# Optimization experiments

Hardware: AMD Instinct MI355X
Metric: run time of the kernel (lower is better)

Reference implementation:

```python
import jax, jax.numpy as jnp
import numpy as np

N, E, D, K = 50000, 600000, 128, 8
EPS = 1e-09


def setup_inputs() -> dict:
    key = jax.random.key(0)
    ks = jax.random.split(key, 10)
    feature = jax.random.normal(ks[0], (N, D), dtype=jnp.float32)
    snorm_n = jax.random.uniform(ks[1], (N, 1), dtype=jnp.float32)
    src = jax.random.randint(ks[2], (E,), 0, N, dtype=jnp.int32)
    dst = jax.random.randint(ks[3], (E,), 0, N, dtype=jnp.int32)
    W_low = jax.random.normal(ks[4], (D, D), dtype=jnp.float32) / np.sqrt(D)
    W_high = jax.random.normal(ks[5], (D, D), dtype=jnp.float32) / np.sqrt(D)
    W_mid = jax.random.normal(ks[6], (D, D), dtype=jnp.float32) / np.sqrt(D)
    gamma_low = jax.random.uniform(ks[7], (K,), dtype=jnp.float32)
    gamma_high = jax.random.uniform(ks[8], (K,), dtype=jnp.float32)
    gamma_mid = jax.random.uniform(ks[9], (K,), dtype=jnp.float32)
    bias = jnp.zeros((D,), dtype=jnp.float32)
    return {"feature": feature, "snorm_n": snorm_n, "src": src, "dst": dst,
            "W_low": W_low, "W_high": W_high, "W_mid": W_mid,
            "gamma_low": gamma_low, "gamma_high": gamma_high,
            "gamma_mid": gamma_mid, "bias": bias}


def _mp(feat, src, dst, norm):
    # symmetric-normalized SpMM: h[v] = norm[v] * sum_{u->v} norm[u]*feat[u]
    msg = (feat * norm[:, None])[src]                        # [E, D] gather
    agg = jax.ops.segment_sum(msg, dst, num_segments=N)       # [N, D] scatter-add
    return agg * norm[:, None]


def reference(feature, snorm_n, src, dst, W_low, W_high, W_mid,
              gamma_low, gamma_high, gamma_mid, bias):
    deg = jax.ops.segment_sum(jnp.ones((E,), feature.dtype), dst, num_segments=N)
    norm = jnp.clip(deg, 1.0) ** -0.5                          # in-degree^-0.5
    alpha = jnp.linspace(EPS, 1.0 - EPS, K).astype(feature.dtype)
    midalpha = jnp.linspace(EPS, 1.0, K).astype(feature.dtype)

    h = _mp(feature, src, dst, norm)

    gl = jax.nn.relu(gamma_low)
    o0 = (jnp.dot(alpha, gl) * h + jnp.dot(1.0 - alpha, gl) * feature) @ W_low.T
    gh = jax.nn.relu(gamma_high)
    o1 = (jnp.dot(-alpha, gh) * h + jnp.dot(1.0 - alpha, gh) * feature) @ W_high.T
    gm = jax.nn.relu(gamma_mid)
    h1 = _mp(h, src, dst, norm)
    o2 = (jnp.sum(gm) * h1 - jnp.dot(midalpha, gm) * feature) @ W_mid.T

    # sequential mutual gating, exactly as the torch in-place updates
    o0 = o0 * jax.nn.sigmoid(o1 + o2)
    o1 = o1 * jax.nn.sigmoid(o0 + o2)
    o2 = o2 * jax.nn.sigmoid(o0 + o1)

    out = o0 + o1 + o2 + bias
    out = out * snorm_n          # graph_norm
    out = jax.nn.relu(out)       # activation
    return out
```

## Files before the change

### kernel.cpp

```cpp
#include <hip/hip_runtime.h>
#include <hip/hip_bf16.h>
#include <math.h>

#define N_NODES 50000
#define N_EDGES 600000
#define DIM 128
#define KGAM 8
#define EPSV 1e-9f

typedef __attribute__((ext_vector_type(8))) short short8;
typedef __attribute__((ext_vector_type(4))) float float4v;

__device__ __forceinline__ float bf2f(short s) {
    unsigned int u = ((unsigned int)(unsigned short)s) << 16;
    return __builtin_bit_cast(float, u);
}
__device__ __forceinline__ short f2bf(float f) {
    return (short)__builtin_bit_cast(unsigned short, __float2bfloat16(f));
}
__device__ __forceinline__ unsigned int pack2(float a, float b) {
    return (unsigned int)(unsigned short)f2bf(a) | ((unsigned int)(unsigned short)f2bf(b) << 16);
}
__device__ __forceinline__ float sigm(float x) { return 1.f / (1.f + __expf(-x)); }
__device__ __forceinline__ float ulo(unsigned int u) { return __builtin_bit_cast(float, u << 16); }
__device__ __forceinline__ float uhi(unsigned int u) { return __builtin_bit_cast(float, u & 0xffff0000u); }

__global__ void k_prep(const float4* __restrict__ feat4,
                       const float* __restrict__ W0, const float* __restrict__ W1,
                       const float* __restrict__ W2,
                       const float* __restrict__ gl, const float* __restrict__ gh,
                       const float* __restrict__ gm,
                       uint4* __restrict__ fb4, unsigned int* __restrict__ Wb,
                       float* __restrict__ coeffs, int* __restrict__ deg) {
    int b = blockIdx.x, tid = threadIdx.x;
    if (b < 3125) {
        int idx = b * 256 + tid;
        if (idx < N_NODES) deg[idx] = 0;
        float4 v0 = feat4[idx * 2];
        float4 v1 = feat4[idx * 2 + 1];
        uint4 o;
        o.x = pack2(v0.x, v0.y); o.y = pack2(v0.z, v0.w);
        o.z = pack2(v1.x, v1.y); o.w = pack2(v1.z, v1.w);
        fb4[idx] = o;
    } else if (b < 3173) {
        int j = (b - 3125) * 256 + tid;
        int g = j >> 12;
        int i = (j & 4095) * 4;
        const float* Ws = (g == 0) ? W0 : (g == 1) ? W1 : W2;
        float4 v = *(const float4*)(Ws + i);
        uint2 o; o.x = pack2(v.x, v.y); o.y = pack2(v.z, v.w);
        *(uint2*)(Wb + (g * DIM * DIM + i) / 2) = o;
    } else if (tid == 0) {
        float a0 = 0, b0 = 0, a1 = 0, b1 = 0, sg = 0, m2 = 0;
        for (int k = 0; k < KGAM; ++k) {
            float al = EPSV + (float)k * (1.f - 2.f * EPSV) / (KGAM - 1);
            float md = EPSV + (float)k * (1.f - EPSV) / (KGAM - 1);
            float l = fmaxf(gl[k], 0.f), h = fmaxf(gh[k], 0.f), m = fmaxf(gm[k], 0.f);
            a0 += al * l;  b0 += (1.f - al) * l;
            a1 += -al * h; b1 += (1.f - al) * h;
            sg += m;       m2 += md * m;
        }
        coeffs[0] = a0; coeffs[1] = b0; coeffs[2] = a1;
        coeffs[3] = b1; coeffs[4] = sg; coeffs[5] = -m2;
    }
}

__global__ void k_deg(const int* __restrict__ dst, int* __restrict__ deg) {
    int e = blockIdx.x * blockDim.x + threadIdx.x;
    if (e < N_EDGES) atomicAdd(&deg[dst[e]], 1);
}

__global__ void k_scan1(const int* __restrict__ deg, int* __restrict__ rowstart,
                        int* __restrict__ bsums, float* __restrict__ norm,
                        int* __restrict__ cnt) {
    __shared__ int s[256];
    int tid = threadIdx.x;
    int i0 = blockIdx.x * 1024 + tid * 4;
    int v[4]; int sum = 0;
#pragma unroll
    for (int c = 0; c < 4; ++c) {
        int i = i0 + c;
        int d = (i < N_NODES) ? deg[i] : 0;
        v[c] = d; sum += d;
    }
    s[tid] = sum; __syncthreads();
#pragma unroll
    for (int off = 1; off < 256; off <<= 1) {
        int t = (tid >= off) ? s[tid - off] : 0;
        __syncthreads();
        s[tid] += t;
        __syncthreads();
    }
    if (tid == 255) bsums[blockIdx.x] = s[255];
    int run = s[tid] - sum;
#pragma unroll
    for (int c = 0; c < 4; ++c) {
        int i = i0 + c;
        if (i < N_NODES) {
            rowstart[i] = run;
            norm[i] = rsqrtf((float)(v[c] < 1 ? 1 : v[c]));
            cnt[i] = 0;
        }
        run += v[c];
    }
}

__global__ void k_scan2(int* __restrict__ bsums, int nb) {
    __shared__ int s[64];
    int tid = threadIdx.x;
    int v = (tid < nb) ? bsums[tid] : 0;
    s[tid] = v; __syncthreads();
#pragma unroll
    for (int off = 1; off < 64; off <<= 1) {
        int t = (tid >= off) ? s[tid - off] : 0;
        __syncthreads();
        s[tid] += t;
        __syncthreads();
    }
    if (tid < nb) bsums[tid] = s[tid] - v;
}

__global__ void k_fill(const int* __restrict__ src, const int* __restrict__ dst,
                       const int* __restrict__ rowstart, const int* __restrict__ bsums,
                       int* __restrict__ cnt, const float* __restrict__ norm,
                       uint2* __restrict__ er) {
    int e = blockIdx.x * blockDim.x + threadIdx.x;
    if (e < N_EDGES) {
        int d = dst[e];
        int slot = rowstart[d] + bsums[d >> 10] + atomicAdd(&cnt[d], 1);
        int u = src[e];
        uint2 rec;
        rec.x = (unsigned int)u;
        rec.y = __builtin_bit_cast(unsigned int, norm[u]);
        er[slot] = rec;
    }
}

__device__ __forceinline__ void acc8(float4v& a0, float4v& a1, uint4 r, float nu) {
    a0.x = fmaf(nu, ulo(r.x), a0.x); a0.y = fmaf(nu, uhi(r.x), a0.y);
    a0.z = fmaf(nu, ulo(r.y), a0.z); a0.w = fmaf(nu, uhi(r.y), a0.w);
    a1.x = fmaf(nu, ulo(r.z), a1.x); a1.y = fmaf(nu, uhi(r.z), a1.y);
    a1.z = fmaf(nu, ulo(r.w), a1.z); a1.w = fmaf(nu, uhi(r.w), a1.w);
}

__global__ __launch_bounds__(512) void k_spmm(
    const uint4* __restrict__ in, const float* __restrict__ norm,
    const int* __restrict__ rowstart, const int* __restrict__ bsums,
    const uint2* __restrict__ er, uint4* __restrict__ out) {
    int node = blockIdx.x * 32 + (threadIdx.x >> 4);
    if (node >= N_NODES) return;
    int gl = threadIdx.x & 15;
    int beg = rowstart[node] + bsums[node >> 10];
    int end = (node == N_NODES - 1) ? N_EDGES
                                    : rowstart[node + 1] + bsums[(node + 1) >> 10];
    float4v a0 = {0.f, 0.f, 0.f, 0.f};
    float4v a1 = {0.f, 0.f, 0.f, 0.f};
    int t = beg;
    for (; t + 3 < end; t += 4) {
        uint2 e0 = er[t], e1 = er[t + 1], e2 = er[t + 2], e3 = er[t + 3];
        uint4 r0 = in[e0.x * 16u + gl];
        uint4 r1 = in[e1.x * 16u + gl];
        uint4 r2 = in[e2.x * 16u + gl];
        uint4 r3 = in[e3.x * 16u + gl];
        acc8(a0, a1, r0, __builtin_bit_cast(float, e0.y));
        acc8(a0, a1, r1, __builtin_bit_cast(float, e1.y));
        acc8(a0, a1, r2, __builtin_bit_cast(float, e2.y));
        acc8(a0, a1, r3, __builtin_bit_cast(float, e3.y));
    }
    for (; t < end; ++t) {
        uint2 e = er[t];
        uint4 r = in[e.x * 16u + gl];
        acc8(a0, a1, r, __builtin_bit_cast(float, e.y));
    }
    float nv = norm[node];
    uint4 o;
    o.x = pack2(a0.x * nv, a0.y * nv); o.y = pack2(a0.z * nv, a0.w * nv);
    o.z = pack2(a1.x * nv, a1.y * nv); o.w = pack2(a1.z * nv, a1.w * nv);
    out[node * 16u + gl] = o;
}

#define RT 64
#define TSTR 136

__global__ __launch_bounds__(512, 4) void k_gemm_fused(
    const short* __restrict__ hB, const short* __restrict__ fB,
    const short* __restrict__ h1B, const short* __restrict__ Wb,
    const float* __restrict__ coeffs, const float* __restrict__ bias,
    const float* __restrict__ snorm, float* __restrict__ out) {
    __shared__ short Ts[3][RT * TSTR];

    const float c0 = coeffs[0], c1 = coeffs[1], c2 = coeffs[2];
    const float c3 = coeffs[3], c4 = coeffs[4], c5 = coeffs[5];
    const int r0 = blockIdx.x * RT;
    const int tid = threadIdx.x;

#pragma unroll
    for (int it = 0; it < 2; ++it) {
        int idx = tid + it * 512;
        int r = idx >> 4;
        int cg = (idx & 15) * 8;
        int row = r0 + r;
        short8 hv = {0,0,0,0,0,0,0,0}, fv = {0,0,0,0,0,0,0,0}, h1v = {0,0,0,0,0,0,0,0};
        if (row < N_NODES) {
            size_t base = (size_t)row * DIM + cg;
            hv  = *(const short8*)(hB + base);
            fv  = *(const short8*)(fB + base);
            h1v = *(const short8*)(h1B + base);
        }
        short8 t0, t1, t2;
#pragma unroll
        for (int j = 0; j < 8; ++j) {
            float hf = bf2f(hv[j]), ff = bf2f(fv[j]), h1f = bf2f(h1v[j]);
            t0[j] = f2bf(c0 * hf + c1 * ff);
            t1[j] = f2bf(c2 * hf + c3 * ff);
            t2[j] = f2bf(c4 * h1f + c5 * ff);
        }
        int la = r * TSTR + cg;
        *(short8*)&Ts[0][la] = t0;
        *(short8*)&Ts[1][la] = t1;
        *(short8*)&Ts[2][la] = t2;
    }
    __syncthreads();

    const int lane = tid & 63;
    const int ct = tid >> 6;
    const int m = lane & 15;
    const int quad = lane >> 4;

    float4v acc[3][4];
    const float4v zero = {0.f, 0.f, 0.f, 0.f};
#pragma unroll
    for (int g = 0; g < 3; ++g)
#pragma unroll
        for (int rt = 0; rt < 4; ++rt) acc[g][rt] = zero;

    const short* wbase = Wb + (ct * 16 + m) * DIM + quad * 8;
#pragma unroll
    for (int ks = 0; ks < 4; ++ks) {
        const short* wp = wbase + ks * 32;
        short8 b0 = *(const short8*)(wp);
        short8 b1 = *(const short8*)(wp + DIM * DIM);
        short8 b2 = *(const short8*)(wp + 2 * DIM * DIM);
#pragma unroll
        for (int rt = 0; rt < 4; ++rt) {
            int aoff = (rt * 16 + m) * TSTR + ks * 32 + quad * 8;
            short8 a0 = *(const short8*)&Ts[0][aoff];
            short8 a1 = *(const short8*)&Ts[1][aoff];
            short8 a2 = *(const short8*)&Ts[2][aoff];
            acc[0][rt] = __builtin_amdgcn_mfma_f32_16x16x32_bf16(a0, b0, acc[0][rt], 0, 0, 0);
            acc[1][rt] = __builtin_amdgcn_mfma_f32_16x16x32_bf16(a1, b1, acc[1][rt], 0, 0, 0);
            acc[2][rt] = __builtin_amdgcn_mfma_f32_16x16x32_bf16(a2, b2, acc[2][rt], 0, 0, 0);
        }
    }

    const int col = ct * 16 + m;
    const float bc = bias[col];
#pragma unroll
    for (int rt = 0; rt < 4; ++rt) {
#pragma unroll
        for (int r = 0; r < 4; ++r) {
            int row = r0 + rt * 16 + quad * 4 + r;
            if (row < N_NODES) {
                float sn = snorm[row];
                float o0 = acc[0][rt][r], o1 = acc[1][rt][r], o2 = acc[2][rt][r];
                float g0 = o0 * sigm(o1 + o2);
                float g1 = o1 * sigm(g0 + o2);
                float g2 = o2 * sigm(g0 + g1);
                float vv = (g0 + g1 + g2 + bc) * sn;
                out[(size_t)row * DIM + col] = fmaxf(vv, 0.f);
            }
        }
    }
}

extern "C" void kernel_launch(void* const* d_in, const int* in_sizes, int n_in,
                              void* d_out, int out_size, void* d_ws, size_t ws_size,
                              hipStream_t stream) {
    const float* feature = (const float*)d_in[0];
    const float* snorm   = (const float*)d_in[1];
    const int*   src     = (const int*)d_in[2];
    const int*   dst     = (const int*)d_in[3];
    const float* W_low   = (const float*)d_in[4];
    const float* W_high  = (const float*)d_in[5];
    const float* W_mid   = (const float*)d_in[6];
    const float* gl      = (const float*)d_in[7];
    const float* gh      = (const float*)d_in[8];
    const float* gm      = (const float*)d_in[9];
    const float* bias    = (const float*)d_in[10];
    float* out = (float*)d_out;

    char* w = (char*)d_ws;
    auto alloc = [&](size_t bytes) {
        char* p = w;
        w += (bytes + 255) & ~(size_t)255;
        return p;
    };
    float* norm   = (float*)alloc((size_t)N_NODES * 4);
    int* deg      = (int*)alloc((size_t)N_NODES * 4);
    int* cnt      = (int*)alloc((size_t)N_NODES * 4);
    int* rowstart = (int*)alloc((size_t)(N_NODES + 1) * 4);
    int* bsums    = (int*)alloc(64 * 4);
    uint2* er     = (uint2*)alloc((size_t)N_EDGES * 8);
    float* coeffs = (float*)alloc(64 * 4);
    short* Wb     = (short*)alloc((size_t)3 * DIM * DIM * 2);
    short* fb     = (short*)alloc((size_t)N_NODES * DIM * 2);
    short* h      = (short*)alloc((size_t)N_NODES * DIM * 2);
    short* h1     = (short*)alloc((size_t)N_NODES * DIM * 2);

    const int nchunks = (N_NODES + 1023) / 1024;

    k_prep<<<3125 + 48 + 1, 256, 0, stream>>>(
        (const float4*)feature, W_low, W_high, W_mid, gl, gh, gm,
        (uint4*)fb, (unsigned int*)Wb, coeffs, deg);
    k_deg<<<(N_EDGES + 255) / 256, 256, 0, stream>>>(dst, deg);
    k_scan1<<<nchunks, 256, 0, stream>>>(deg, rowstart, bsums, norm, cnt);
    k_scan2<<<1, 64, 0, stream>>>(bsums, nchunks);
    k_fill<<<(N_EDGES + 255) / 256, 256, 0, stream>>>(src, dst, rowstart, bsums,
                                                      cnt, norm, er);
    int spmm_blocks = (N_NODES + 31) / 32;
    k_spmm<<<spmm_blocks, 512, 0, stream>>>((const uint4*)fb, norm, rowstart, bsums,
                                            er, (uint4*)h);
    k_spmm<<<spmm_blocks, 512, 0, stream>>>((const uint4*)h, norm, rowstart, bsums,
                                            er, (uint4*)h1);
    k_gemm_fused<<<(N_NODES + RT - 1) / RT, 512, 0, stream>>>(
        h, fb, h1, Wb, coeffs, bias, snorm, out);
}
```

Before: 240.0 us.

## Merge degree count into prep, single-pass scan, and deepen SpMM unroll

```diff
diff --git a/kernel.cpp b/kernel.cpp
--- a/kernel.cpp
+++ b/kernel.cpp
@@ -8,6 +8,9 @@
 #define KGAM 8
 #define EPSV 1e-9f
 
+#define CHUNK_SHIFT 11
+#define NCHUNKS 25
+
 typedef __attribute__((ext_vector_type(8))) short short8;
 typedef __attribute__((ext_vector_type(4))) float float4v;
 
@@ -25,17 +28,17 @@
 __device__ __forceinline__ float ulo(unsigned int u) { return __builtin_bit_cast(float, u << 16); }
 __device__ __forceinline__ float uhi(unsigned int u) { return __builtin_bit_cast(float, u & 0xffff0000u); }
 
-__global__ void k_prep(const float4* __restrict__ feat4,
-                       const float* __restrict__ W0, const float* __restrict__ W1,
-                       const float* __restrict__ W2,
-                       const float* __restrict__ gl, const float* __restrict__ gh,
-                       const float* __restrict__ gm,
-                       uint4* __restrict__ fb4, unsigned int* __restrict__ Wb,
-                       float* __restrict__ coeffs, int* __restrict__ deg) {
+__global__ void k_prep_deg(const float4* __restrict__ feat4,
+                           const float* __restrict__ W0, const float* __restrict__ W1,
+                           const float* __restrict__ W2,
+                           const float* __restrict__ gl, const float* __restrict__ gh,
+                           const float* __restrict__ gm,
+                           const int* __restrict__ dst,
+                           uint4* __restrict__ fb4, unsigned int* __restrict__ Wb,
+                           float* __restrict__ coeffs, int* __restrict__ deg) {
     int b = blockIdx.x, tid = threadIdx.x;
     if (b < 3125) {
         int idx = b * 256 + tid;
-        if (idx < N_NODES) deg[idx] = 0;
         float4 v0 = feat4[idx * 2];
         float4 v1 = feat4[idx * 2 + 1];
         uint4 o;
@@ -50,32 +53,36 @@
         float4 v = *(const float4*)(Ws + i);
         uint2 o; o.x = pack2(v.x, v.y); o.y = pack2(v.z, v.w);
         *(uint2*)(Wb + (g * DIM * DIM + i) / 2) = o;
-    } else if (tid == 0) {
-        float a0 = 0, b0 = 0, a1 = 0, b1 = 0, sg = 0, m2 = 0;
-        for (int k = 0; k < KGAM; ++k) {
-            float al = EPSV + (float)k * (1.f - 2.f * EPSV) / (KGAM - 1);
-            float md = EPSV + (float)k * (1.f - EPSV) / (KGAM - 1);
-            float l = fmaxf(gl[k], 0.f), h = fmaxf(gh[k], 0.f), m = fmaxf(gm[k], 0.f);
-            a0 += al * l;  b0 += (1.f - al) * l;
-            a1 += -al * h; b1 += (1.f - al) * h;
-            sg += m;       m2 += md * m;
-        }
-        coeffs[0] = a0; coeffs[1] = b0; coeffs[2] = a1;
-        coeffs[3] = b1; coeffs[4] = sg; coeffs[5] = -m2;
-    }
-}
-
-__global__ void k_deg(const int* __restrict__ dst, int* __restrict__ deg) {
-    int e = blockIdx.x * blockDim.x + threadIdx.x;
-    if (e < N_EDGES) atomicAdd(&deg[dst[e]], 1);
-}
-
-__global__ void k_scan1(const int* __restrict__ deg, int* __restrict__ rowstart,
-                        int* __restrict__ bsums, float* __restrict__ norm,
-                        int* __restrict__ cnt) {
-    __shared__ int s[256];
+    } else if (b == 3173) {
+        if (tid == 0) {
+            float a0 = 0, b0 = 0, a1 = 0, b1 = 0, sg = 0, m2 = 0;
+            for (int k = 0; k < KGAM; ++k) {
+                float al = EPSV + (float)k * (1.f - 2.f * EPSV) / (KGAM - 1);
+                float md = EPSV + (float)k * (1.f - EPSV) / (KGAM - 1);
+                float l = fmaxf(gl[k], 0.f), h = fmaxf(gh[k], 0.f), m = fmaxf(gm[k], 0.f);
+                a0 += al * l;  b0 += (1.f - al) * l;
+                a1 += -al * h; b1 += (1.f - al) * h;
+                sg += m;       m2 += md * m;
+            }
+            coeffs[0] = a0; coeffs[1] = b0; coeffs[2] = a1;
+            coeffs[3] = b1; coeffs[4] = sg; coeffs[5] = -m2;
+        }
+    } else {
+        int e = (b - 3174) * 256 + tid;
+        if (e < N_EDGES) atomicAdd(&deg[dst[e]], 1);
+    }
+}
+
+__global__ __launch_bounds__(512) void k_scan(const int* __restrict__ deg,
+                                              int* __restrict__ rowstart,
+                                              int* __restrict__ bsums,
+                                              float* __restrict__ norm,
+                                              int* __restrict__ done) {
+    __shared__ int s[512];
+    __shared__ int lastf;
+    __shared__ int bs[NCHUNKS];
     int tid = threadIdx.x;
-    int i0 = blockIdx.x * 1024 + tid * 4;
+    int i0 = blockIdx.x * 2048 + tid * 4;
     int v[4]; int sum = 0;
 #pragma unroll
     for (int c = 0; c < 4; ++c) {
@@ -85,13 +92,13 @@
     }
     s[tid] = sum; __syncthreads();
 #pragma unroll
-    for (int off = 1; off < 256; off <<= 1) {
+    for (int off = 1; off < 512; off <<= 1) {
         int t = (tid >= off) ? s[tid - off] : 0;
         __syncthreads();
         s[tid] += t;
         __syncthreads();
     }
-    if (tid == 255) bsums[blockIdx.x] = s[255];
+    if (tid == 511) bsums[blockIdx.x] = s[511];
     int run = s[tid] - sum;
 #pragma unroll
     for (int c = 0; c < 4; ++c) {
@@ -99,25 +106,27 @@
         if (i < N_NODES) {
             rowstart[i] = run;
             norm[i] = rsqrtf((float)(v[c] < 1 ? 1 : v[c]));
-            cnt[i] = 0;
         }
         run += v[c];
     }
-}
-
-__global__ void k_scan2(int* __restrict__ bsums, int nb) {
-    __shared__ int s[64];
-    int tid = threadIdx.x;
-    int v = (tid < nb) ? bsums[tid] : 0;
-    s[tid] = v; __syncthreads();
-#pragma unroll
-    for (int off = 1; off < 64; off <<= 1) {
-        int t = (tid >= off) ? s[tid - off] : 0;
+    __threadfence();
+    __syncthreads();
+    if (tid == 0) {
+        int old = atomicAdd(done, 1);
+        lastf = (old == (int)gridDim.x - 1) ? 1 : 0;
+    }
+    __syncthreads();
+    if (lastf) {
+        __threadfence();
+        if (tid < NCHUNKS) bs[tid] = bsums[tid];
         __syncthreads();
-        s[tid] += t;
+        if (tid == 0) {
+            int run2 = 0;
+            for (int i = 0; i < NCHUNKS; ++i) { int t = bs[i]; bs[i] = run2; run2 += t; }
+        }
         __syncthreads();
-    }
-    if (tid < nb) bsums[tid] = s[tid] - v;
+        if (tid < NCHUNKS) bsums[tid] = bs[tid];
+    }
 }
 
 __global__ void k_fill(const int* __restrict__ src, const int* __restrict__ dst,
@@ -127,7 +136,7 @@
     int e = blockIdx.x * blockDim.x + threadIdx.x;
     if (e < N_EDGES) {
         int d = dst[e];
-        int slot = rowstart[d] + bsums[d >> 10] + atomicAdd(&cnt[d], 1);
+        int slot = rowstart[d] + bsums[d >> CHUNK_SHIFT] + atomicAdd(&cnt[d], 1);
         int u = src[e];
         uint2 rec;
         rec.x = (unsigned int)u;
@@ -143,20 +152,41 @@
     a1.z = fmaf(nu, ulo(r.w), a1.z); a1.w = fmaf(nu, uhi(r.w), a1.w);
 }
 
-__global__ __launch_bounds__(512) void k_spmm(
+__global__ __launch_bounds__(256, 6) void k_spmm(
     const uint4* __restrict__ in, const float* __restrict__ norm,
     const int* __restrict__ rowstart, const int* __restrict__ bsums,
     const uint2* __restrict__ er, uint4* __restrict__ out) {
-    int node = blockIdx.x * 32 + (threadIdx.x >> 4);
+    int node = blockIdx.x * 16 + (threadIdx.x >> 4);
     if (node >= N_NODES) return;
     int gl = threadIdx.x & 15;
-    int beg = rowstart[node] + bsums[node >> 10];
-    int end = (node == N_NODES - 1) ? N_EDGES
-                                    : rowstart[node + 1] + bsums[(node + 1) >> 10];
+    int beg = rowstart[node] + bsums[node >> CHUNK_SHIFT];
+    int end = (node == N_NODES - 1)
+                  ? N_EDGES
+                  : rowstart[node + 1] + bsums[(node + 1) >> CHUNK_SHIFT];
     float4v a0 = {0.f, 0.f, 0.f, 0.f};
     float4v a1 = {0.f, 0.f, 0.f, 0.f};
     int t = beg;
-    for (; t + 3 < end; t += 4) {
+    for (; t + 7 < end; t += 8) {
+        uint2 e0 = er[t],     e1 = er[t + 1], e2 = er[t + 2], e3 = er[t + 3];
+        uint2 e4 = er[t + 4], e5 = er[t + 5], e6 = er[t + 6], e7 = er[t + 7];
+        uint4 r0 = in[e0.x * 16u + gl];
+        uint4 r1 = in[e1.x * 16u + gl];
+        uint4 r2 = in[e2.x * 16u + gl];
+        uint4 r3 = in[e3.x * 16u + gl];
+        uint4 r4 = in[e4.x * 16u + gl];
+        uint4 r5 = in[e5.x * 16u + gl];
+        uint4 r6 = in[e6.x * 16u + gl];
+        uint4 r7 = in[e7.x * 16u + gl];
+        acc8(a0, a1, r0, __builtin_bit_cast(float, e0.y));
+        acc8(a0, a1, r1, __builtin_bit_cast(float, e1.y));
+        acc8(a0, a1, r2, __builtin_bit_cast(float, e2.y));
+        acc8(a0, a1, r3, __builtin_bit_cast(float, e3.y));
+        acc8(a0, a1, r4, __builtin_bit_cast(float, e4.y));
+        acc8(a0, a1, r5, __builtin_bit_cast(float, e5.y));
+        acc8(a0, a1, r6, __builtin_bit_cast(float, e6.y));
+        acc8(a0, a1, r7, __builtin_bit_cast(float, e7.y));
+    }
+    if (t + 3 < end) {
         uint2 e0 = er[t], e1 = er[t + 1], e2 = er[t + 2], e3 = er[t + 3];
         uint4 r0 = in[e0.x * 16u + gl];
         uint4 r1 = in[e1.x * 16u + gl];
@@ -166,6 +196,7 @@
         acc8(a0, a1, r1, __builtin_bit_cast(float, e1.y));
         acc8(a0, a1, r2, __builtin_bit_cast(float, e2.y));
         acc8(a0, a1, r3, __builtin_bit_cast(float, e3.y));
+        t += 4;
     }
     for (; t < end; ++t) {
         uint2 e = er[t];
@@ -295,9 +326,11 @@
         w += (bytes + 255) & ~(size_t)255;
         return p;
     };
-    float* norm   = (float*)alloc((size_t)N_NODES * 4);
     int* deg      = (int*)alloc((size_t)N_NODES * 4);
     int* cnt      = (int*)alloc((size_t)N_NODES * 4);
+    int* done     = (int*)alloc(256);
+    size_t zero_bytes = (size_t)((char*)done - (char*)deg) + 256;
+    float* norm   = (float*)alloc((size_t)N_NODES * 4);
     int* rowstart = (int*)alloc((size_t)(N_NODES + 1) * 4);
     int* bsums    = (int*)alloc(64 * 4);
     uint2* er     = (uint2*)alloc((size_t)N_EDGES * 8);
@@ -307,20 +340,17 @@
     short* h      = (short*)alloc((size_t)N_NODES * DIM * 2);
     short* h1     = (short*)alloc((size_t)N_NODES * DIM * 2);
 
-    const int nchunks = (N_NODES + 1023) / 1024;
-
-    k_prep<<<3125 + 48 + 1, 256, 0, stream>>>(
-        (const float4*)feature, W_low, W_high, W_mid, gl, gh, gm,
+    hipMemsetAsync(deg, 0, zero_bytes, stream);
+    k_prep_deg<<<3174 + 2344, 256, 0, stream>>>(
+        (const float4*)feature, W_low, W_high, W_mid, gl, gh, gm, dst,
         (uint4*)fb, (unsigned int*)Wb, coeffs, deg);
-    k_deg<<<(N_EDGES + 255) / 256, 256, 0, stream>>>(dst, deg);
-    k_scan1<<<nchunks, 256, 0, stream>>>(deg, rowstart, bsums, norm, cnt);
-    k_scan2<<<1, 64, 0, stream>>>(bsums, nchunks);
+    k_scan<<<NCHUNKS, 512, 0, stream>>>(deg, rowstart, bsums, norm, done);
     k_fill<<<(N_EDGES + 255) / 256, 256, 0, stream>>>(src, dst, rowstart, bsums,
                                                       cnt, norm, er);
-    int spmm_blocks = (N_NODES + 31) / 32;
-    k_spmm<<<spmm_blocks, 512, 0, stream>>>((const uint4*)fb, norm, rowstart, bsums,
+    int spmm_blocks = (N_NODES + 15) / 16;
+    k_spmm<<<spmm_blocks, 256, 0, stream>>>((const uint4*)fb, norm, rowstart, bsums,
                                             er, (uint4*)h);
-    k_spmm<<<spmm_blocks, 512, 0, stream>>>((const uint4*)h, norm, rowstart, bsums,
+    k_spmm<<<spmm_blocks, 256, 0, stream>>>((const uint4*)h, norm, rowstart, bsums,
                                             er, (uint4*)h1);
     k_gemm_fused<<<(N_NODES + RT - 1) / RT, 512, 0, stream>>>(
         h, fb, h1, Wb, coeffs, bias, snorm, out);
```

Measured after the change: 242.8 us. About the same (+1.2%).
